# Performance work log

Hardware: AMD Instinct MI355X
Metric: run time of the kernel (lower is better)

Reference implementation:

```python
import jax, jax.numpy as jnp
import numpy as np

N = 100000      # nodes
E = 1600000     # edges (avg degree 16)
DIM = 128       # node_input_dim == node_hidden_dim
H = 8           # num_heads
D = DIM // H    # per-head out_feats = 16
NEG_SLOPE_ATTN = 0.2   # DGL GATConv attention LeakyReLU
NEG_SLOPE_ACT = 0.01   # F.leaky_relu default (inter-layer activation)


def _leaky(x, s):
    return jnp.where(x >= 0, x, s * x)


def setup_inputs() -> dict:
    key = jax.random.key(0)
    ks = jax.random.split(key, 12)
    s = 0.1
    return {
        "n_feat": jax.random.normal(ks[0], (N, DIM), jnp.float32),
        "src": jax.random.randint(ks[1], (E,), 0, N, dtype=jnp.int32),
        "dst": jax.random.randint(ks[2], (E,), 0, N, dtype=jnp.int32),
        # layer 0 params
        "W0": jax.random.normal(ks[3], (DIM, DIM), jnp.float32) * s,
        "al0": jax.random.normal(ks[4], (H, D), jnp.float32) * s,
        "ar0": jax.random.normal(ks[5], (H, D), jnp.float32) * s,
        "b0": jnp.zeros((DIM,), jnp.float32),
        # layer 1 params
        "W1": jax.random.normal(ks[6], (DIM, DIM), jnp.float32) * s,
        "al1": jax.random.normal(ks[7], (H, D), jnp.float32) * s,
        "ar1": jax.random.normal(ks[8], (H, D), jnp.float32) * s,
        "b1": jnp.zeros((DIM,), jnp.float32),
    }


def gat_layer(h, src, dst, W, al, ar, b, apply_act):
    # h: [N, DIM] -> feat: [N, H, D]
    feat = (h @ W).reshape(N, H, D)
    el = jnp.einsum('nhd,hd->nh', feat, al)   # [N, H]
    er = jnp.einsum('nhd,hd->nh', feat, ar)   # [N, H]
    # per-edge attention logits with LeakyReLU(0.2)
    e = _leaky(el[src] + er[dst], NEG_SLOPE_ATTN)         # [E, H]
    # edge-softmax over incoming edges of each dst node (numerically stable)
    m = jax.ops.segment_max(e, dst, num_segments=N)       # [N, H]
    ee = jnp.exp(e - m[dst])                              # [E, H]
    denom = jax.ops.segment_sum(ee, dst, num_segments=N)  # [N, H]
    a = ee / denom[dst]                                   # [E, H]
    # weighted message aggregation (scatter-add to dst)
    msg = feat[src] * a[:, :, None]                       # [E, H, D]
    rst = jax.ops.segment_sum(msg, dst, num_segments=N)   # [N, H, D]
    # residual (identity since in_feats == num_heads*out_feats) + bias
    rst = rst + h.reshape(N, H, D) + b.reshape(1, H, D)
    if apply_act:
        rst = _leaky(rst, NEG_SLOPE_ACT)
    return rst.reshape(N, H * D)


def reference(n_feat, src, dst, W0, al0, ar0, b0, W1, al1, ar1, b1):
    h = gat_layer(n_feat, src, dst, W0, al0, ar0, b0, apply_act=True)
    h = gat_layer(h, src, dst, W1, al1, ar1, b1, apply_act=False)
    return h
```

## Files before the change

### kernel.cpp

```cpp
#include <hip/hip_runtime.h>
#include <hip/hip_bf16.h>

#define HGAT 8
#define DIMGAT 128
#define CAPB 4608

typedef __attribute__((ext_vector_type(8))) short short8;
typedef __attribute__((ext_vector_type(4))) float f32x4;

__device__ __forceinline__ float bf16_to_f32(unsigned int u16) {
    return __uint_as_float(u16 << 16);
}
__device__ __forceinline__ unsigned short f32_to_bf16(float x) {
    unsigned int b = __float_as_uint(x);
    b += 0x7FFFu + ((b >> 16) & 1u);
    return (unsigned short)(b >> 16);
}

__global__ void initb_kernel(int* __restrict__ bcursor, int nb) {
    int i = blockIdx.x * blockDim.x + threadIdx.x;
    if (i < nb) bcursor[i] = i * CAPB;
}

__global__ __launch_bounds__(256)
void bucket_scatter(const int* __restrict__ src, const int* __restrict__ dst,
                    int* __restrict__ bcursor, unsigned int* __restrict__ bucket_arr,
                    int e, int nb) {
    __shared__ int lcnt[400];
    __shared__ int lbase[400];
    __shared__ int lrank[400];
    int t = threadIdx.x;
    int e0 = blockIdx.x * 4096;
    for (int i = t; i < nb; i += 256) { lcnt[i] = 0; lrank[i] = 0; }
    __syncthreads();
    int myb[16]; int mys[16];
    #pragma unroll
    for (int q = 0; q < 16; ++q) {
        int i = e0 + q * 256 + t;
        int bb = -1, ss = 0;
        if (i < e) {
            int d = dst[i];
            bb = d >> 8;
            ss = (src[i] << 8) | (d & 255);
        }
        myb[q] = bb; mys[q] = ss;
        if (bb >= 0) atomicAdd(&lcnt[bb], 1);
    }
    __syncthreads();
    for (int i = t; i < nb; i += 256) {
        int c = lcnt[i];
        lbase[i] = c ? atomicAdd(&bcursor[i], c) : 0;
    }
    __syncthreads();
    #pragma unroll
    for (int q = 0; q < 16; ++q) {
        int bb = myb[q];
        if (bb >= 0) {
            int r = atomicAdd(&lrank[bb], 1);
            int pos = lbase[bb] + r;
            if (pos < (bb + 1) * CAPB)
                bucket_arr[pos] = (unsigned int)mys[q];
        }
    }
}

__global__ __launch_bounds__(256)
void bucket_finalize(const unsigned int* __restrict__ bucket_arr,
                     const int* __restrict__ bcursor, int* __restrict__ col_src,
                     int* __restrict__ start, int* __restrict__ deg, int n) {
    __shared__ int lcnt[256];
    __shared__ int lcur[256];
    int b = blockIdx.x;
    int t = threadIdx.x;
    int base = b * CAPB;
    int cnt_b = bcursor[b] - base;
    lcnt[t] = 0;
    __syncthreads();
    for (int i = t; i < cnt_b; i += 256)
        atomicAdd(&lcnt[bucket_arr[base + i] & 255u], 1);
    __syncthreads();
    int my = lcnt[t];
    for (int off = 1; off < 256; off <<= 1) {
        int v = (t >= off) ? lcnt[t - off] : 0;
        __syncthreads();
        lcnt[t] += v;
        __syncthreads();
    }
    int excl = lcnt[t] - my;
    int node = b * 256 + t;
    if (node < n) {
        start[node] = base + excl;
        deg[node] = my;
    }
    lcur[t] = excl;
    __syncthreads();
    for (int i = t; i < cnt_b; i += 256) {
        unsigned int p = bucket_arr[base + i];
        int r = atomicAdd(&lcur[p & 255u], 1);
        col_src[base + r] = (int)(p >> 8);
    }
}

__global__ void wcvt_kernel(const float* __restrict__ W0, const float* __restrict__ W1,
                            unsigned short* __restrict__ Wb0, unsigned short* __restrict__ Wb1) {
    int t = blockIdx.x * blockDim.x + threadIdx.x;
    const float* W = (t < 2048) ? W0 : W1;
    unsigned short* Wb = (t < 2048) ? Wb0 : Wb1;
    int tt = t & 2047;
    int lane = tt & 63;
    int ct = (tt >> 6) & 7;
    int ks = tt >> 9;
    int lr = lane & 15, lg = lane >> 4;
    const float* wp = W + (ks * 32 + lg * 8) * 128 + ct * 16 + lr;
    unsigned short o[8];
    #pragma unroll
    for (int j = 0; j < 8; ++j) o[j] = f32_to_bf16(wp[j * 128]);
    *(uint4*)(Wb + (size_t)tt * 8) = *(const uint4*)o;
}

template<int AIN>
__global__ __launch_bounds__(256)
void gemm_mfma_kernel(const void* __restrict__ A_, const unsigned short* __restrict__ Wb,
                      unsigned short* __restrict__ Cb,
                      const float* __restrict__ al, const float* __restrict__ ar,
                      float* __restrict__ el, float* __restrict__ er, int nrows) {
    int wave = (int)((blockIdx.x * (size_t)blockDim.x + threadIdx.x) >> 6);
    int nwaves = (int)((gridDim.x * (size_t)blockDim.x) >> 6);
    int lane = threadIdx.x & 63;
    int lr = lane & 15;
    int lg = lane >> 4;

    const short8* wb8 = (const short8*)Wb;
    short8 bfrag[4][8];
    #pragma unroll
    for (int ks = 0; ks < 4; ++ks)
        #pragma unroll
        for (int ct = 0; ct < 8; ++ct)
            bfrag[ks][ct] = wb8[(ks * 8 + ct) * 64 + lane];

    float alv[8], arv[8];
    #pragma unroll
    for (int ct = 0; ct < 8; ++ct) {
        alv[ct] = al[ct * 16 + lr];
        arv[ct] = ar[ct * 16 + lr];
    }

    int ntiles = nrows >> 4;
    for (int t = wave; t < ntiles; t += nwaves) {
        f32x4 acc[8];
        #pragma unroll
        for (int ct = 0; ct < 8; ++ct) acc[ct] = (f32x4){0.f, 0.f, 0.f, 0.f};
        #pragma unroll
        for (int ks = 0; ks < 4; ++ks) {
            short8 af;
            if (AIN == 0) {
                const float* ap = (const float*)A_ + (size_t)(t * 16 + lr) * 128 + lg * 8 + ks * 32;
                float4 a0 = *(const float4*)ap;
                float4 a1 = *(const float4*)(ap + 4);
                af[0] = (short)f32_to_bf16(a0.x); af[1] = (short)f32_to_bf16(a0.y);
                af[2] = (short)f32_to_bf16(a0.z); af[3] = (short)f32_to_bf16(a0.w);
                af[4] = (short)f32_to_bf16(a1.x); af[5] = (short)f32_to_bf16(a1.y);
                af[6] = (short)f32_to_bf16(a1.z); af[7] = (short)f32_to_bf16(a1.w);
            } else {
                const unsigned short* ap = (const unsigned short*)A_ + (size_t)(t * 16 + lr) * 128 + lg * 8 + ks * 32;
                af = *(const short8*)ap;
            }
            #pragma unroll
            for (int ct = 0; ct < 8; ++ct)
                acc[ct] = __builtin_amdgcn_mfma_f32_16x16x32_bf16(af, bfrag[ks][ct], acc[ct], 0, 0, 0);
        }
        unsigned short* cp = Cb + (size_t)(t * 16 + lg * 4) * 128 + lr;
        #pragma unroll
        for (int ct = 0; ct < 8; ++ct) {
            #pragma unroll
            for (int r = 0; r < 4; ++r)
                cp[(size_t)r * 128 + ct * 16] = f32_to_bf16(acc[ct][r]);
        }
        #pragma unroll
        for (int r = 0; r < 4; ++r) {
            int row = t * 16 + lg * 4 + r;
            #pragma unroll
            for (int ct = 0; ct < 8; ++ct) {
                float vl = acc[ct][r] * alv[ct];
                float vr = acc[ct][r] * arv[ct];
                #pragma unroll
                for (int off = 1; off < 16; off <<= 1) {
                    vl += __shfl_xor(vl, off, 64);
                    vr += __shfl_xor(vr, off, 64);
                }
                if (lr == 0) {
                    el[(size_t)row * 8 + ct] = vl;
                    er[(size_t)row * 8 + ct] = vr;
                }
            }
        }
    }
}

template<int HINB, int OUTB, int ACT>
__global__ __launch_bounds__(256)
void agg_kernel(const unsigned short* __restrict__ featb, const float* __restrict__ el,
                const float* __restrict__ er, const int* __restrict__ col_src,
                const int* __restrict__ start_arr, const int* __restrict__ deg,
                const void* __restrict__ hin_, const float* __restrict__ bias,
                void* __restrict__ out_, int n) {
    int wid = (int)((blockIdx.x * (size_t)blockDim.x + threadIdx.x) >> 6);
    if (wid >= n) return;
    int lane = threadIdx.x & 63;
    int h = lane >> 3;
    int jbase = lane & 0x38;
    int start = start_arr[wid];
    int end = start + deg[wid];
    float er_own = er[wid * 8 + h];

    float sum = 0.f, ax = 0.f, ay = 0.f;
    const unsigned int* featw = (const unsigned int*)featb;
    int i = start;
    for (; i + 8 <= end; i += 8) {
        int s_own = col_src[i + (lane & 7)];
        float q = el[s_own * 8 + h] + er_own;
        q = (q >= 0.f) ? q : 0.2f * q;
        float p_own = __expf(q);
        #pragma unroll
        for (int j = 0; j < 8; ++j) {
            int sj   = __shfl(s_own, jbase + j);
            float pj = __shfl(p_own, jbase + j);
            sum += pj;
            unsigned int fw = featw[(size_t)sj * 64 + lane];
            ax = fmaf(pj, bf16_to_f32(fw & 0xFFFFu), ax);
            ay = fmaf(pj, bf16_to_f32(fw >> 16), ay);
        }
    }
    for (; i < end; ++i) {
        int s = col_src[i];
        float e = el[s * 8 + h] + er_own;
        e = (e >= 0.f) ? e : 0.2f * e;
        float p = __expf(e);
        sum += p;
        unsigned int fw = featw[(size_t)s * 64 + lane];
        ax = fmaf(p, bf16_to_f32(fw & 0xFFFFu), ax);
        ay = fmaf(p, bf16_to_f32(fw >> 16), ay);
    }
    float inv = (end > start) ? 1.f / sum : 0.f;
    float hx, hy;
    if (HINB) {
        unsigned int hw = ((const unsigned int*)hin_)[(size_t)wid * 64 + lane];
        hx = bf16_to_f32(hw & 0xFFFFu);
        hy = bf16_to_f32(hw >> 16);
    } else {
        float2 hv = ((const float2*)hin_)[(size_t)wid * 64 + lane];
        hx = hv.x; hy = hv.y;
    }
    float2 bv = ((const float2*)bias)[lane];
    float ox = fmaf(ax, inv, hx + bv.x);
    float oy = fmaf(ay, inv, hy + bv.y);
    if (ACT) {
        ox = (ox >= 0.f) ? ox : 0.01f * ox;
        oy = (oy >= 0.f) ? oy : 0.01f * oy;
    }
    if (OUTB) {
        unsigned int pw = (unsigned int)f32_to_bf16(ox) | ((unsigned int)f32_to_bf16(oy) << 16);
        ((unsigned int*)out_)[(size_t)wid * 64 + lane] = pw;
    } else {
        ((float2*)out_)[(size_t)wid * 64 + lane] = make_float2(ox, oy);
    }
}

extern "C" void kernel_launch(void* const* d_in, const int* in_sizes, int n_in,
                              void* d_out, int out_size, void* d_ws, size_t ws_size,
                              hipStream_t stream) {
    const float* n_feat = (const float*)d_in[0];
    const int*   src    = (const int*)d_in[1];
    const int*   dst    = (const int*)d_in[2];
    const float* W0  = (const float*)d_in[3];
    const float* al0 = (const float*)d_in[4];
    const float* ar0 = (const float*)d_in[5];
    const float* b0  = (const float*)d_in[6];
    const float* W1  = (const float*)d_in[7];
    const float* al1 = (const float*)d_in[8];
    const float* ar1 = (const float*)d_in[9];
    const float* b1  = (const float*)d_in[10];

    const int n = in_sizes[0] / DIMGAT;
    const int e = in_sizes[1];
    const int nb = (n + 255) >> 8;

    char* ws = (char*)d_ws;
    size_t off = 0;
    auto alloc = [&](size_t bytes) {
        void* p = ws + off;
        off += (bytes + 255) & ~(size_t)255;
        return p;
    };
    int* bcursor = (int*)alloc((size_t)nb * 4);
    int* start   = (int*)alloc((size_t)n * 4);
    int* deg     = (int*)alloc((size_t)n * 4);
    unsigned int* bucket_arr = (unsigned int*)alloc((size_t)nb * CAPB * 4);
    int* col_src = (int*)alloc((size_t)nb * CAPB * 4);
    float* el    = (float*)alloc((size_t)n * HGAT * 4);
    float* er    = (float*)alloc((size_t)n * HGAT * 4);
    unsigned short* featb = (unsigned short*)alloc((size_t)n * DIMGAT * 2);
    unsigned short* Wb0   = (unsigned short*)alloc((size_t)DIMGAT * DIMGAT * 2);
    unsigned short* Wb1   = (unsigned short*)alloc((size_t)DIMGAT * DIMGAT * 2);
    size_t off_noh1 = off;
    unsigned short* h1b   = (unsigned short*)alloc((size_t)n * DIMGAT * 2);
    const bool useB = (off <= ws_size);
    (void)off_noh1;

    float* out = (float*)d_out;

    initb_kernel<<<(nb + 255) / 256, 256, 0, stream>>>(bcursor, nb);
    bucket_scatter<<<(e + 4095) / 4096, 256, 0, stream>>>(src, dst, bcursor,
                                                          bucket_arr, e, nb);
    bucket_finalize<<<nb, 256, 0, stream>>>(bucket_arr, bcursor, col_src,
                                            start, deg, n);
    wcvt_kernel<<<16, 256, 0, stream>>>(W0, W1, Wb0, Wb1);

    const int gemm_grid = 1024;
    const int agg_grid  = (n * 64 + 255) / 256;

    if (useB) {
        gemm_mfma_kernel<0><<<gemm_grid, 256, 0, stream>>>(n_feat, Wb0, featb,
                                                           al0, ar0, el, er, n);
        agg_kernel<0, 1, 1><<<agg_grid, 256, 0, stream>>>(featb, el, er, col_src,
                                                          start, deg, n_feat, b0, h1b, n);
        gemm_mfma_kernel<1><<<gemm_grid, 256, 0, stream>>>(h1b, Wb1, featb,
                                                           al1, ar1, el, er, n);
        agg_kernel<1, 0, 0><<<agg_grid, 256, 0, stream>>>(featb, el, er, col_src,
                                                          start, deg, h1b, b1, out, n);
    } else {
        gemm_mfma_kernel<0><<<gemm_grid, 256, 0, stream>>>(n_feat, Wb0, featb,
                                                           al0, ar0, el, er, n);
        agg_kernel<0, 0, 1><<<agg_grid, 256, 0, stream>>>(featb, el, er, col_src,
                                                          start, deg, n_feat, b0, out, n);
        gemm_mfma_kernel<0><<<gemm_grid, 256, 0, stream>>>(out, Wb1, featb,
                                                           al1, ar1, el, er, n);
        agg_kernel<0, 0, 0><<<agg_grid, 256, 0, stream>>>(featb, el, er, col_src,
                                                          start, deg, out, b1, out, n);
    }
}
```

Before: 399.2 us.

## Fold attention vectors into weights and batch neighbor feature loads in aggregation

Precomputes W·al and W·ar per head as an extra 16-column bf16 weight block, so the GEMM produces el/er with one additional MFMA per k-step. This replaces the per-row shuffle-reduction epilogue that used many cross-lane shuffles. The aggregation loop now issues all eight neighbor feature loads before consuming them, and handles the tail with masked lanes instead of a scalar remainder loop, to raise memory-level parallelism. The folded weights are rounded to bf16, which changes the precision of the attention logits.

```diff
diff --git a/kernel.cpp b/kernel.cpp
--- a/kernel.cpp
+++ b/kernel.cpp
@@ -102,27 +102,53 @@
 }
 
 __global__ void wcvt_kernel(const float* __restrict__ W0, const float* __restrict__ W1,
-                            unsigned short* __restrict__ Wb0, unsigned short* __restrict__ Wb1) {
+                            const float* __restrict__ al0, const float* __restrict__ ar0,
+                            const float* __restrict__ al1, const float* __restrict__ ar1,
+                            unsigned short* __restrict__ Wb0, unsigned short* __restrict__ Wb1,
+                            unsigned short* __restrict__ Wba0, unsigned short* __restrict__ Wba1) {
     int t = blockIdx.x * blockDim.x + threadIdx.x;
-    const float* W = (t < 2048) ? W0 : W1;
-    unsigned short* Wb = (t < 2048) ? Wb0 : Wb1;
-    int tt = t & 2047;
-    int lane = tt & 63;
-    int ct = (tt >> 6) & 7;
-    int ks = tt >> 9;
-    int lr = lane & 15, lg = lane >> 4;
-    const float* wp = W + (ks * 32 + lg * 8) * 128 + ct * 16 + lr;
-    unsigned short o[8];
-    #pragma unroll
-    for (int j = 0; j < 8; ++j) o[j] = f32_to_bf16(wp[j * 128]);
-    *(uint4*)(Wb + (size_t)tt * 8) = *(const uint4*)o;
+    if (t < 4096) {
+        const float* W = (t < 2048) ? W0 : W1;
+        unsigned short* Wb = (t < 2048) ? Wb0 : Wb1;
+        int tt = t & 2047;
+        int lane = tt & 63;
+        int ct = (tt >> 6) & 7;
+        int ks = tt >> 9;
+        int lr = lane & 15, lg = lane >> 4;
+        const float* wp = W + (ks * 32 + lg * 8) * 128 + ct * 16 + lr;
+        unsigned short o[8];
+        #pragma unroll
+        for (int j = 0; j < 8; ++j) o[j] = f32_to_bf16(wp[j * 128]);
+        *(uint4*)(Wb + (size_t)tt * 8) = *(const uint4*)o;
+    } else {
+        int t2 = t - 4096;
+        int layer = t2 >> 8;
+        int r = t2 & 255;
+        int ks = r >> 6, lane = r & 63;
+        int lr = lane & 15, lg = lane >> 4;
+        const float* W  = layer ? W1 : W0;
+        const float* av = (lr < 8) ? (layer ? al1 : al0) : (layer ? ar1 : ar0);
+        unsigned short* Wba = layer ? Wba1 : Wba0;
+        int hh = lr & 7;
+        unsigned short o[8];
+        #pragma unroll
+        for (int j = 0; j < 8; ++j) {
+            int k = ks * 32 + lg * 8 + j;
+            float v = 0.f;
+            #pragma unroll
+            for (int d = 0; d < 16; ++d)
+                v = fmaf(W[(size_t)k * 128 + hh * 16 + d], av[hh * 16 + d], v);
+            o[j] = f32_to_bf16(v);
+        }
+        *(uint4*)(Wba + (size_t)(ks * 64 + lane) * 8) = *(const uint4*)o;
+    }
 }
 
 template<int AIN>
 __global__ __launch_bounds__(256)
 void gemm_mfma_kernel(const void* __restrict__ A_, const unsigned short* __restrict__ Wb,
+                      const unsigned short* __restrict__ Wba,
                       unsigned short* __restrict__ Cb,
-                      const float* __restrict__ al, const float* __restrict__ ar,
                       float* __restrict__ el, float* __restrict__ er, int nrows) {
     int wave = (int)((blockIdx.x * (size_t)blockDim.x + threadIdx.x) >> 6);
     int nwaves = (int)((gridDim.x * (size_t)blockDim.x) >> 6);
@@ -130,24 +156,22 @@
     int lr = lane & 15;
     int lg = lane >> 4;
 
-    const short8* wb8 = (const short8*)Wb;
+    const short8* wb8  = (const short8*)Wb;
+    const short8* wba8 = (const short8*)Wba;
     short8 bfrag[4][8];
+    short8 bfragA[4];
     #pragma unroll
-    for (int ks = 0; ks < 4; ++ks)
+    for (int ks = 0; ks < 4; ++ks) {
         #pragma unroll
         for (int ct = 0; ct < 8; ++ct)
             bfrag[ks][ct] = wb8[(ks * 8 + ct) * 64 + lane];
-
-    float alv[8], arv[8];
-    #pragma unroll
-    for (int ct = 0; ct < 8; ++ct) {
-        alv[ct] = al[ct * 16 + lr];
-        arv[ct] = ar[ct * 16 + lr];
+        bfragA[ks] = wba8[ks * 64 + lane];
     }
 
     int ntiles = nrows >> 4;
     for (int t = wave; t < ntiles; t += nwaves) {
         f32x4 acc[8];
+        f32x4 accA = (f32x4){0.f, 0.f, 0.f, 0.f};
         #pragma unroll
         for (int ct = 0; ct < 8; ++ct) acc[ct] = (f32x4){0.f, 0.f, 0.f, 0.f};
         #pragma unroll
@@ -168,6 +192,7 @@
             #pragma unroll
             for (int ct = 0; ct < 8; ++ct)
                 acc[ct] = __builtin_amdgcn_mfma_f32_16x16x32_bf16(af, bfrag[ks][ct], acc[ct], 0, 0, 0);
+            accA = __builtin_amdgcn_mfma_f32_16x16x32_bf16(af, bfragA[ks], accA, 0, 0, 0);
         }
         unsigned short* cp = Cb + (size_t)(t * 16 + lg * 4) * 128 + lr;
         #pragma unroll
@@ -176,23 +201,12 @@
             for (int r = 0; r < 4; ++r)
                 cp[(size_t)r * 128 + ct * 16] = f32_to_bf16(acc[ct][r]);
         }
+        float* basep = (lr < 8) ? el : er;
+        int hh = lr & 7;
         #pragma unroll
         for (int r = 0; r < 4; ++r) {
             int row = t * 16 + lg * 4 + r;
-            #pragma unroll
-            for (int ct = 0; ct < 8; ++ct) {
-                float vl = acc[ct][r] * alv[ct];
-                float vr = acc[ct][r] * arv[ct];
-                #pragma unroll
-                for (int off = 1; off < 16; off <<= 1) {
-                    vl += __shfl_xor(vl, off, 64);
-                    vr += __shfl_xor(vr, off, 64);
-                }
-                if (lr == 0) {
-                    el[(size_t)row * 8 + ct] = vl;
-                    er[(size_t)row * 8 + ct] = vr;
-                }
-            }
+            basep[(size_t)row * 8 + hh] = accA[r];
         }
     }
 }
@@ -208,6 +222,7 @@
     if (wid >= n) return;
     int lane = threadIdx.x & 63;
     int h = lane >> 3;
+    int jsub = lane & 7;
     int jbase = lane & 0x38;
     int start = start_arr[wid];
     int end = start + deg[wid];
@@ -215,31 +230,29 @@
 
     float sum = 0.f, ax = 0.f, ay = 0.f;
     const unsigned int* featw = (const unsigned int*)featb;
-    int i = start;
-    for (; i + 8 <= end; i += 8) {
-        int s_own = col_src[i + (lane & 7)];
+    for (int i = start; i < end; i += 8) {
+        int idx = i + jsub;
+        bool valid = idx < end;
+        int s_own = col_src[valid ? idx : end - 1];
         float q = el[s_own * 8 + h] + er_own;
         q = (q >= 0.f) ? q : 0.2f * q;
-        float p_own = __expf(q);
+        float p_own = valid ? __expf(q) : 0.f;
+        int sj[8]; float pj[8];
         #pragma unroll
         for (int j = 0; j < 8; ++j) {
-            int sj   = __shfl(s_own, jbase + j);
-            float pj = __shfl(p_own, jbase + j);
-            sum += pj;
-            unsigned int fw = featw[(size_t)sj * 64 + lane];
-            ax = fmaf(pj, bf16_to_f32(fw & 0xFFFFu), ax);
-            ay = fmaf(pj, bf16_to_f32(fw >> 16), ay);
-        }
-    }
-    for (; i < end; ++i) {
-        int s = col_src[i];
-        float e = el[s * 8 + h] + er_own;
-        e = (e >= 0.f) ? e : 0.2f * e;
-        float p = __expf(e);
-        sum += p;
-        unsigned int fw = featw[(size_t)s * 64 + lane];
-        ax = fmaf(p, bf16_to_f32(fw & 0xFFFFu), ax);
-        ay = fmaf(p, bf16_to_f32(fw >> 16), ay);
+            sj[j] = __shfl(s_own, jbase + j);
+            pj[j] = __shfl(p_own, jbase + j);
+        }
+        unsigned int fw[8];
+        #pragma unroll
+        for (int j = 0; j < 8; ++j)
+            fw[j] = featw[(size_t)sj[j] * 64 + lane];
+        #pragma unroll
+        for (int j = 0; j < 8; ++j) {
+            sum += pj[j];
+            ax = fmaf(pj[j], bf16_to_f32(fw[j] & 0xFFFFu), ax);
+            ay = fmaf(pj[j], bf16_to_f32(fw[j] >> 16), ay);
+        }
     }
     float inv = (end > start) ? 1.f / sum : 0.f;
     float hx, hy;
@@ -302,10 +315,10 @@
     unsigned short* featb = (unsigned short*)alloc((size_t)n * DIMGAT * 2);
     unsigned short* Wb0   = (unsigned short*)alloc((size_t)DIMGAT * DIMGAT * 2);
     unsigned short* Wb1   = (unsigned short*)alloc((size_t)DIMGAT * DIMGAT * 2);
-    size_t off_noh1 = off;
+    unsigned short* Wba0  = (unsigned short*)alloc((size_t)4 * 64 * 8 * 2);
+    unsigned short* Wba1  = (unsigned short*)alloc((size_t)4 * 64 * 8 * 2);
     unsigned short* h1b   = (unsigned short*)alloc((size_t)n * DIMGAT * 2);
     const bool useB = (off <= ws_size);
-    (void)off_noh1;
 
     float* out = (float*)d_out;
 
@@ -314,27 +327,28 @@
                                                           bucket_arr, e, nb);
     bucket_finalize<<<nb, 256, 0, stream>>>(bucket_arr, bcursor, col_src,
                                             start, deg, n);
-    wcvt_kernel<<<16, 256, 0, stream>>>(W0, W1, Wb0, Wb1);
+    wcvt_kernel<<<18, 256, 0, stream>>>(W0, W1, al0, ar0, al1, ar1,
+                                        Wb0, Wb1, Wba0, Wba1);
 
     const int gemm_grid = 1024;
     const int agg_grid  = (n * 64 + 255) / 256;
 
     if (useB) {
-        gemm_mfma_kernel<0><<<gemm_grid, 256, 0, stream>>>(n_feat, Wb0, featb,
-                                                           al0, ar0, el, er, n);
+        gemm_mfma_kernel<0><<<gemm_grid, 256, 0, stream>>>(n_feat, Wb0, Wba0, featb,
+                                                           el, er, n);
         agg_kernel<0, 1, 1><<<agg_grid, 256, 0, stream>>>(featb, el, er, col_src,
                                                           start, deg, n_feat, b0, h1b, n);
-        gemm_mfma_kernel<1><<<gemm_grid, 256, 0, stream>>>(h1b, Wb1, featb,
-                                                           al1, ar1, el, er, n);
+        gemm_mfma_kernel<1><<<gemm_grid, 256, 0, stream>>>(h1b, Wb1, Wba1, featb,
+                                                           el, er, n);
         agg_kernel<1, 0, 0><<<agg_grid, 256, 0, stream>>>(featb, el, er, col_src,
                                                           start, deg, h1b, b1, out, n);
     } else {
-        gemm_mfma_kernel<0><<<gemm_grid, 256, 0, stream>>>(n_feat, Wb0, featb,
-                                                           al0, ar0, el, er, n);
+        gemm_mfma_kernel<0><<<gemm_grid, 256, 0, stream>>>(n_feat, Wb0, Wba0, featb,
+                                                           el, er, n);
         agg_kernel<0, 0, 1><<<agg_grid, 256, 0, stream>>>(featb, el, er, col_src,
                                                           start, deg, n_feat, b0, out, n);
-        gemm_mfma_kernel<0><<<gemm_grid, 256, 0, stream>>>(out, Wb1, featb,
-                                                           al1, ar1, el, er, n);
+        gemm_mfma_kernel<0><<<gemm_grid, 256, 0, stream>>>(out, Wb1, Wba1, featb,
+                                                           el, er, n);
         agg_kernel<0, 0, 0><<<agg_grid, 256, 0, stream>>>(featb, el, er, col_src,
                                                           start, deg, out, b1, out, n);
     }
```

After: 362.3 us. -9.2%, faster.
